# Optimization experiments

Hardware: AMD Instinct MI355X
Metric: run time of the kernel (lower is better)

Reference implementation:

```python
import jax, jax.numpy as jnp
import numpy as np

B, C, H, W = 16, 256, 32, 32
NUM_LAYERS = 30
OUT = 16  # sqrt(out_channels)
EPS = 1e-5


def setup_inputs() -> dict:
    key = jax.random.key(0)
    k1, k2, k3 = jax.random.split(key, 3)
    x = jax.random.normal(k1, (B, C, H, W), dtype=jnp.float32)
    # delta_t ~ small positive values (module inits ~N(0.01, 0.005))
    delta_t = jax.random.uniform(k2, (NUM_LAYERS, 1), dtype=jnp.float32) * 0.02
    matrices = jax.random.normal(k3, (NUM_LAYERS, 1, 1, OUT, OUT), dtype=jnp.float32) * 0.1
    gamma = jnp.ones((H * W,), dtype=jnp.float32)   # BatchNorm2d weight, oc = i*i = H*W
    beta = jnp.zeros((H * W,), dtype=jnp.float32)   # BatchNorm2d bias
    return {"x": x, "delta_t": delta_t, "matrices": matrices, "gamma": gamma, "beta": beta}


def _bn_relu6(z, gamma, beta):
    # training-mode BatchNorm2d over channel axis 1 (channels = H*W), then ReLU6
    mean = jnp.mean(z, axis=(0, 2, 3), keepdims=True)
    var = jnp.mean(jnp.square(z - mean), axis=(0, 2, 3), keepdims=True)  # biased var
    zhat = (z - mean) * jax.lax.rsqrt(var + EPS)
    g = gamma.reshape(1, -1, 1, 1)
    b = beta.reshape(1, -1, 1, 1)
    return jnp.clip(zhat * g + b, 0.0, 6.0)


def reference(x, delta_t, matrices, gamma, beta):
    b, c, h, w = x.shape
    hw = h * w
    # feature_reshape: [B,C,H,W] -> [B,HW,C] -> [B,HW,out,out] (inn == out branch)
    x1 = x.reshape(b, c, hw).transpose(0, 2, 1).reshape(b, hw, OUT, OUT)
    dt = jnp.clip(delta_t, 0.0, 6.0)[:, 0]  # relu6(delta_t), shape [L]

    def step(y0, params):
        m, dtl = params  # m: [1,1,out,out] broadcasts elementwise against x1
        dydt = -y0 + _bn_relu6(y0 + m * x1, gamma, beta)
        return y0 + dtl * dydt, None

    y0, _ = jax.lax.scan(step, x1, (matrices, dt))
    # (y0 + x1): [B, HW, out, out] -> view [B,H,W,out*out] -> permute to [B,out*out,H,W]
    y = (y0 + x1).reshape(b, h, w, OUT * OUT).transpose(0, 3, 1, 2)
    return y
```

## Files before the change

kernel.cpp:

```cpp
#include <hip/hip_runtime.h>

typedef float v2f __attribute__((ext_vector_type(2)));
typedef float v4f __attribute__((ext_vector_type(4)));

#define HW      1024
#define NROWS   4096
#define NLAYERS 30
#define TPB     256

static __device__ __forceinline__ v2f pk_fma(v2f a, v2f b, v2f c) {
    v2f d; asm("v_pk_fma_f32 %0, %1, %2, %3" : "=v"(d) : "v"(a), "v"(b), "v"(c));
    return d;
}
static __device__ __forceinline__ v2f pk_add(v2f a, v2f b) {
    v2f d; asm("v_pk_add_f32 %0, %1, %2" : "=v"(d) : "v"(a), "v"(b));
    return d;
}

template <int CTRL, int RMASK>
__device__ __forceinline__ float dpp_add(float x) {
    int t = __builtin_amdgcn_update_dpp(0, __builtin_bit_cast(int, x),
                                        CTRL, RMASK, 0xf, true);
    return x + __builtin_bit_cast(float, t);
}
__device__ __forceinline__ float wave_sum64(float x) {
    x = dpp_add<0x111, 0xf>(x);
    x = dpp_add<0x112, 0xf>(x);
    x = dpp_add<0x114, 0xf>(x);
    x = dpp_add<0x118, 0xf>(x);
    x = dpp_add<0x142, 0xa>(x);
    x = dpp_add<0x143, 0xc>(x);
    return x;
}

__global__ __launch_bounds__(TPB) void txp64(const float* __restrict__ src,
                                             float* __restrict__ dst,
                                             int M, int N) {
    __shared__ float tile[64][65];
    const int n0 = blockIdx.x * 64;
    const int m0 = blockIdx.y * 64;
    const int tx = threadIdx.x & 63;
    const int ty = threadIdx.x >> 6;
#pragma unroll
    for (int i = 0; i < 16; ++i) {
        const int r = ty + 4 * i;
        tile[r][tx] = src[(size_t)(m0 + r) * N + n0 + tx];
    }
    __syncthreads();
#pragma unroll
    for (int i = 0; i < 16; ++i) {
        const int r = ty + 4 * i;
        dst[(size_t)(n0 + r) * M + m0 + tx] = tile[tx][r];
    }
}

__global__ __launch_bounds__(TPB, 4) void ode_z4w(
    float* ws, const float* __restrict__ delta_t,
    const float* __restrict__ matrices, const float* __restrict__ gamma,
    const float* __restrict__ beta) {

    const int p    = blockIdx.x;
    const int t    = threadIdx.x;
    const int wid  = t >> 6;
    const int lane = t & 63;
    const int c0   = (4 * t) & 255;
    float* row = ws + (size_t)p * NROWS;

    __shared__ float xs[NROWS];
    __shared__ __align__(16) v2f red[2][4];

    const float gp = gamma[p];
    const float bp = beta[p];

    v2f z[8];
    v2f s0 = {0.f, 0.f}, s1 = {0.f, 0.f}, q0 = {0.f, 0.f}, q1 = {0.f, 0.f};

    {
        const v4f m4 = *(const v4f*)(matrices + c0);
        const v2f mA = {m4.x, m4.y}, mB = {m4.z, m4.w};
#pragma unroll
        for (int j = 0; j < 4; ++j) {
            const v4f x4 = *(const v4f*)(row + 4 * t + 1024 * j);
            *(v4f*)&xs[4 * t + 1024 * j] = x4;
            const v2f xA = {x4.x, x4.y}, xB = {x4.z, x4.w};
            z[2 * j]     = pk_fma(mA, xA, xA);
            z[2 * j + 1] = pk_fma(mB, xB, xB);
            s0 = pk_add(s0, z[2 * j]);
            q0 = pk_fma(z[2 * j], z[2 * j], q0);
            s1 = pk_add(s1, z[2 * j + 1]);
            q1 = pk_fma(z[2 * j + 1], z[2 * j + 1], q1);
        }
        const v2f sv = pk_add(s0, s1);
        const v2f qv = pk_add(q0, q1);
        const float ss = wave_sum64(sv.x + sv.y);
        const float qq = wave_sum64(qv.x + qv.y);
        if (lane == 63) red[0][wid] = (v2f){ss, qq};
    }

    v4f   mqc = *(const v4f*)(matrices + c0);
    v4f   mqn = *(const v4f*)(matrices + 256 + c0);
    float dtc = delta_t[0];
    float dtn = delta_t[1];
    __syncthreads();

    for (int k = 0; k < NLAYERS - 1; ++k) {
        const int k2 = (k + 2 < NLAYERS) ? k + 2 : NLAYERS - 1;
        const v4f   mq2   = *(const v4f*)(matrices + k2 * 256 + c0);
        const float dt_nn = delta_t[k2];

        const int par = k & 1;
        const v4f r0 = *(const v4f*)&red[par][0];
        const v4f r1 = *(const v4f*)&red[par][2];
        const float S = (r0.x + r0.z) + (r1.x + r1.z);
        const float Q = (r0.y + r0.w) + (r1.y + r1.w);

        const float dtk  = __builtin_amdgcn_fmed3f(dtc, 0.0f, 6.0f);
        const float mean = S * (1.0f / 4096.0f);
        const float var  = fmaf(-mean, mean, Q * (1.0f / 4096.0f));
        const float rstd = rsqrtf(var + 1e-5f);
        const float g    = gp * rstd;
        const float b    = fmaf(-mean, g, bp);
        const float om   = 1.0f - dtk;
        const float gd   = g * dtk;
        const float bd   = b * dtk;
        const float hi   = 6.0f * dtk;
        const v2f gd2 = {gd, gd}, bd2 = {bd, bd};
        const v2f om2 = {om, om};
        const v2f omn = {-om, -om};
        const v2f mcA = {mqc.x, mqc.y}, mcB = {mqc.z, mqc.w};
        const v2f mnA = {mqn.x, mqn.y}, mnB = {mqn.z, mqn.w};
        const v2f dmA = pk_fma(omn, mcA, mnA);
        const v2f dmB = pk_fma(omn, mcB, mnB);

        s0 = (v2f){0.f, 0.f}; s1 = (v2f){0.f, 0.f};
        q0 = (v2f){0.f, 0.f}; q1 = (v2f){0.f, 0.f};

#pragma unroll
        for (int j = 0; j < 4; ++j) {
            const v4f x4 = *(const v4f*)&xs[4 * t + 1024 * j];
            const v2f xA = {x4.x, x4.y}, xB = {x4.z, x4.w};
            {
                const int e = 2 * j;
                v2f a = pk_fma(z[e], gd2, bd2);
                a.x = __builtin_amdgcn_fmed3f(a.x, 0.0f, hi);
                a.y = __builtin_amdgcn_fmed3f(a.y, 0.0f, hi);
                v2f u = pk_fma(dmA, xA, a);
                z[e] = pk_fma(om2, z[e], u);
                s0 = pk_add(s0, z[e]);
                q0 = pk_fma(z[e], z[e], q0);
            }
            {
                const int e = 2 * j + 1;
                v2f a = pk_fma(z[e], gd2, bd2);
                a.x = __builtin_amdgcn_fmed3f(a.x, 0.0f, hi);
                a.y = __builtin_amdgcn_fmed3f(a.y, 0.0f, hi);
                v2f u = pk_fma(dmB, xB, a);
                z[e] = pk_fma(om2, z[e], u);
                s1 = pk_add(s1, z[e]);
                q1 = pk_fma(z[e], z[e], q1);
            }
        }
        const v2f sv = pk_add(s0, s1);
        const v2f qv = pk_add(q0, q1);
        const float ss = wave_sum64(sv.x + sv.y);
        const float qq = wave_sum64(qv.x + qv.y);
        if (lane == 63) red[par ^ 1][wid] = (v2f){ss, qq};

        mqc = mqn; mqn = mq2; dtc = dtn; dtn = dt_nn;
        __syncthreads();
    }

    {
        const v4f r0 = *(const v4f*)&red[(NLAYERS - 1) & 1][0];
        const v4f r1 = *(const v4f*)&red[(NLAYERS - 1) & 1][2];
        const float S = (r0.x + r0.z) + (r1.x + r1.z);
        const float Q = (r0.y + r0.w) + (r1.y + r1.w);

        const float dtk  = __builtin_amdgcn_fmed3f(dtc, 0.0f, 6.0f);
        const float mean = S * (1.0f / 4096.0f);
        const float var  = fmaf(-mean, mean, Q * (1.0f / 4096.0f));
        const float rstd = rsqrtf(var + 1e-5f);
        const float g    = gp * rstd;
        const float b    = fmaf(-mean, g, bp);
        const float om   = 1.0f - dtk;
        const float gd   = g * dtk;
        const float bd   = b * dtk;
        const float hi   = 6.0f * dtk;
        const v2f gd2 = {gd, gd}, bd2 = {bd, bd};
        const v2f om2 = {om, om};
        const v2f omn = {-om, -om};
        const v2f one2 = {1.0f, 1.0f};
        const v2f mcA = {mqc.x, mqc.y}, mcB = {mqc.z, mqc.w};
        const v2f dmA = pk_fma(omn, mcA, one2);
        const v2f dmB = pk_fma(omn, mcB, one2);

#pragma unroll
        for (int j = 0; j < 4; ++j) {
            const v4f x4 = *(const v4f*)&xs[4 * t + 1024 * j];
            const v2f xA = {x4.x, x4.y}, xB = {x4.z, x4.w};
            v2f o0, o1;
            {
                const int e = 2 * j;
                v2f a = pk_fma(z[e], gd2, bd2);
                a.x = __builtin_amdgcn_fmed3f(a.x, 0.0f, hi);
                a.y = __builtin_amdgcn_fmed3f(a.y, 0.0f, hi);
                v2f u = pk_fma(dmA, xA, a);
                o0 = pk_fma(om2, z[e], u);
            }
            {
                const int e = 2 * j + 1;
                v2f a = pk_fma(z[e], gd2, bd2);
                a.x = __builtin_amdgcn_fmed3f(a.x, 0.0f, hi);
                a.y = __builtin_amdgcn_fmed3f(a.y, 0.0f, hi);
                v2f u = pk_fma(dmB, xB, a);
                o1 = pk_fma(om2, z[e], u);
            }
            v4f o4; o4.x = o0.x; o4.y = o0.y; o4.z = o1.x; o4.w = o1.y;
            *(v4f*)(row + 4 * t + 1024 * j) = o4;
        }
    }
}

__global__ __launch_bounds__(TPB) void ode_fused(const float* __restrict__ x,
                                                 const float* __restrict__ delta_t,
                                                 const float* __restrict__ matrices,
                                                 const float* __restrict__ gamma,
                                                 const float* __restrict__ beta,
                                                 float* __restrict__ out) {
    const int bid = blockIdx.x;
    const int p   = ((bid & 7) << 7) | (bid >> 3);
    const int t   = threadIdx.x;

    __shared__ float smat[(NLAYERS + 1) * 256];
    __shared__ float sdt[NLAYERS];
    __shared__ __align__(16) v2f red[2][4];

#pragma unroll
    for (int i = 0; i < NLAYERS; ++i)
        smat[i * 256 + t] = matrices[i * 256 + t];
    if (t < NLAYERS)
        sdt[t] = __builtin_amdgcn_fmed3f(delta_t[t], 0.0f, 6.0f);

    v2f x1[8], y[8];
#pragma unroll
    for (int k = 0; k < 8; ++k) {
        x1[k].x = x[(size_t)(t + 512 * k) * HW + p];
        x1[k].y = x[(size_t)(t + 512 * k + 256) * HW + p];
        y[k] = x1[k];
    }

    const float gp   = gamma[p];
    const float bp   = beta[p];
    const int   wid  = t >> 6;
    const int   lane = t & 63;

    __syncthreads();
    float m_cur = smat[t];

    for (int l = 0; l < NLAYERS; ++l) {
        const float dtl = sdt[l];
        const v2f m2    = {m_cur, m_cur};
        const v2f dt2   = {dtl, dtl};
        const v2f om2   = {1.0f - dtl, 1.0f - dtl};

        v2f z[8];
        v2f sA = {0.f, 0.f}, sB = {0.f, 0.f};
        v2f qA = {0.f, 0.f}, qB = {0.f, 0.f};
#pragma unroll
        for (int k = 0; k < 8; k += 2) {
            z[k]     = __builtin_elementwise_fma(m2, x1[k], y[k]);
            z[k + 1] = __builtin_elementwise_fma(m2, x1[k + 1], y[k + 1]);
            sA += z[k];
            sB += z[k + 1];
            qA = __builtin_elementwise_fma(z[k], z[k], qA);
            qB = __builtin_elementwise_fma(z[k + 1], z[k + 1], qB);
        }
#pragma unroll
        for (int k = 0; k < 8; ++k) y[k] *= om2;

        const v2f sv = sA + sB;
        const v2f qv = qA + qB;
        float s = wave_sum64(sv.x + sv.y);
        float q = wave_sum64(qv.x + qv.y);

        const int par = l & 1;
        if (lane == 63) { v2f w; w.x = s; w.y = q; red[par][wid] = w; }
        m_cur = smat[(l + 1) * 256 + t];
        __syncthreads();

        const float4 r0 = *(const float4*)&red[par][0];
        const float4 r1 = *(const float4*)&red[par][2];
        const float S  = (r0.x + r0.z) + (r1.x + r1.z);
        const float S2 = (r0.y + r0.w) + (r1.y + r1.w);

        const float mean = S * (1.0f / 4096.0f);
        const float var  = fmaf(-mean, mean, S2 * (1.0f / 4096.0f));
        const float rstd = rsqrtf(var + 1e-5f);
        const float g    = gp * rstd;
        const float bb   = fmaf(-mean, g, bp);
        const v2f g2 = {g, g}, b2 = {bb, bb};
        const v2f z0 = {0.f, 0.f}, s6 = {6.f, 6.f};
#pragma unroll
        for (int k = 0; k < 8; ++k) {
            v2f a = __builtin_elementwise_fma(z[k], g2, b2);
            a = __builtin_elementwise_max(a, z0);
            a = __builtin_elementwise_min(a, s6);
            y[k] = __builtin_elementwise_fma(dt2, a, y[k]);
        }
    }

#pragma unroll
    for (int k = 0; k < 8; ++k) {
        out[(size_t)(t + 512 * k) * HW + p]       = y[k].x + x1[k].x;
        out[(size_t)(t + 512 * k + 256) * HW + p] = y[k].y + x1[k].y;
    }
}

extern "C" void kernel_launch(void* const* d_in, const int* in_sizes, int n_in,
                              void* d_out, int out_size, void* d_ws, size_t ws_size,
                              hipStream_t stream) {
    const float* x        = (const float*)d_in[0];
    const float* delta_t  = (const float*)d_in[1];
    const float* matrices = (const float*)d_in[2];
    const float* gamma    = (const float*)d_in[3];
    const float* beta     = (const float*)d_in[4];
    float* out = (float*)d_out;

    const size_t need = (size_t)HW * NROWS * sizeof(float);
    if (d_ws != nullptr && ws_size >= need) {
        float* ws = (float*)d_ws;
        txp64<<<dim3(HW / 64, NROWS / 64), dim3(TPB), 0, stream>>>(x, ws, NROWS, HW);
        ode_z4w<<<dim3(HW), dim3(TPB), 0, stream>>>(ws, delta_t, matrices, gamma, beta);
        txp64<<<dim3(NROWS / 64, HW / 64), dim3(TPB), 0, stream>>>(ws, out, HW, NROWS);
    } else {
        ode_fused<<<dim3(HW), dim3(TPB), 0, stream>>>(x, delta_t, matrices, gamma, beta, out);
    }
}
```

Baseline: 119.7 us.

## Run each BN channel's ODE in a single wavefront with register-resident state

The per-channel ODE kernel now uses one 64-lane wavefront per channel instead of four waves. Each lane keeps 64 state values and 64 input values in registers rather than staging x in LDS. The batch-norm statistics are reduced with DPP plus readlane, which removes the per-layer __syncthreads and LDS exchange. The cost is a much larger register footprint and only 1024 single-wave blocks, so occupancy and latency hiding drop and per-lane serial work per layer is four times larger.

```diff
diff --git a/kernel.cpp b/kernel.cpp
--- a/kernel.cpp
+++ b/kernel.cpp
@@ -32,6 +32,10 @@
     x = dpp_add<0x143, 0xc>(x);
     return x;
 }
+__device__ __forceinline__ float bcast63(float x) {
+    return __builtin_bit_cast(float,
+        __builtin_amdgcn_readlane(__builtin_bit_cast(int, x), 63));
+}
 
 __global__ __launch_bounds__(TPB) void txp64(const float* __restrict__ src,
                                              float* __restrict__ dst,
@@ -54,35 +58,30 @@
     }
 }
 
-__global__ __launch_bounds__(TPB, 4) void ode_z4w(
-    float* ws, const float* __restrict__ delta_t,
+__global__ __launch_bounds__(64, 1) void ode_zreg(
+    float* __restrict__ ws, const float* __restrict__ delta_t,
     const float* __restrict__ matrices, const float* __restrict__ gamma,
     const float* __restrict__ beta) {
 
     const int p    = blockIdx.x;
-    const int t    = threadIdx.x;
-    const int wid  = t >> 6;
-    const int lane = t & 63;
-    const int c0   = (4 * t) & 255;
+    const int lane = threadIdx.x;
+    const int c0   = 4 * lane;
     float* row = ws + (size_t)p * NROWS;
-
-    __shared__ float xs[NROWS];
-    __shared__ __align__(16) v2f red[2][4];
 
     const float gp = gamma[p];
     const float bp = beta[p];
 
-    v2f z[8];
+    v4f xr[16];
+    v2f z[32];
     v2f s0 = {0.f, 0.f}, s1 = {0.f, 0.f}, q0 = {0.f, 0.f}, q1 = {0.f, 0.f};
 
     {
         const v4f m4 = *(const v4f*)(matrices + c0);
         const v2f mA = {m4.x, m4.y}, mB = {m4.z, m4.w};
 #pragma unroll
-        for (int j = 0; j < 4; ++j) {
-            const v4f x4 = *(const v4f*)(row + 4 * t + 1024 * j);
-            *(v4f*)&xs[4 * t + 1024 * j] = x4;
-            const v2f xA = {x4.x, x4.y}, xB = {x4.z, x4.w};
+        for (int j = 0; j < 16; ++j) {
+            xr[j] = *(const v4f*)(row + 4 * lane + 256 * j);
+            const v2f xA = {xr[j].x, xr[j].y}, xB = {xr[j].z, xr[j].w};
             z[2 * j]     = pk_fma(mA, xA, xA);
             z[2 * j + 1] = pk_fma(mB, xB, xB);
             s0 = pk_add(s0, z[2 * j]);
@@ -90,29 +89,27 @@
             s1 = pk_add(s1, z[2 * j + 1]);
             q1 = pk_fma(z[2 * j + 1], z[2 * j + 1], q1);
         }
-        const v2f sv = pk_add(s0, s1);
-        const v2f qv = pk_add(q0, q1);
-        const float ss = wave_sum64(sv.x + sv.y);
-        const float qq = wave_sum64(qv.x + qv.y);
-        if (lane == 63) red[0][wid] = (v2f){ss, qq};
     }
 
     v4f   mqc = *(const v4f*)(matrices + c0);
     v4f   mqn = *(const v4f*)(matrices + 256 + c0);
     float dtc = delta_t[0];
     float dtn = delta_t[1];
-    __syncthreads();
 
     for (int k = 0; k < NLAYERS - 1; ++k) {
+        asm volatile("" : "+v"(xr[0]), "+v"(xr[1]), "+v"(xr[2]), "+v"(xr[3]));
+        asm volatile("" : "+v"(xr[4]), "+v"(xr[5]), "+v"(xr[6]), "+v"(xr[7]));
+        asm volatile("" : "+v"(xr[8]), "+v"(xr[9]), "+v"(xr[10]), "+v"(xr[11]));
+        asm volatile("" : "+v"(xr[12]), "+v"(xr[13]), "+v"(xr[14]), "+v"(xr[15]));
+
         const int k2 = (k + 2 < NLAYERS) ? k + 2 : NLAYERS - 1;
         const v4f   mq2   = *(const v4f*)(matrices + k2 * 256 + c0);
         const float dt_nn = delta_t[k2];
 
-        const int par = k & 1;
-        const v4f r0 = *(const v4f*)&red[par][0];
-        const v4f r1 = *(const v4f*)&red[par][2];
-        const float S = (r0.x + r0.z) + (r1.x + r1.z);
-        const float Q = (r0.y + r0.w) + (r1.y + r1.w);
+        const v2f sv = pk_add(s0, s1);
+        const v2f qv = pk_add(q0, q1);
+        const float S = bcast63(wave_sum64(sv.x + sv.y));
+        const float Q = bcast63(wave_sum64(qv.x + qv.y));
 
         const float dtk  = __builtin_amdgcn_fmed3f(dtc, 0.0f, 6.0f);
         const float mean = S * (1.0f / 4096.0f);
@@ -136,9 +133,8 @@
         q0 = (v2f){0.f, 0.f}; q1 = (v2f){0.f, 0.f};
 
 #pragma unroll
-        for (int j = 0; j < 4; ++j) {
-            const v4f x4 = *(const v4f*)&xs[4 * t + 1024 * j];
-            const v2f xA = {x4.x, x4.y}, xB = {x4.z, x4.w};
+        for (int j = 0; j < 16; ++j) {
+            const v2f xA = {xr[j].x, xr[j].y}, xB = {xr[j].z, xr[j].w};
             {
                 const int e = 2 * j;
                 v2f a = pk_fma(z[e], gd2, bd2);
@@ -160,21 +156,15 @@
                 q1 = pk_fma(z[e], z[e], q1);
             }
         }
+
+        mqc = mqn; mqn = mq2; dtc = dtn; dtn = dt_nn;
+    }
+
+    {
         const v2f sv = pk_add(s0, s1);
         const v2f qv = pk_add(q0, q1);
-        const float ss = wave_sum64(sv.x + sv.y);
-        const float qq = wave_sum64(qv.x + qv.y);
-        if (lane == 63) red[par ^ 1][wid] = (v2f){ss, qq};
-
-        mqc = mqn; mqn = mq2; dtc = dtn; dtn = dt_nn;
-        __syncthreads();
-    }
-
-    {
-        const v4f r0 = *(const v4f*)&red[(NLAYERS - 1) & 1][0];
-        const v4f r1 = *(const v4f*)&red[(NLAYERS - 1) & 1][2];
-        const float S = (r0.x + r0.z) + (r1.x + r1.z);
-        const float Q = (r0.y + r0.w) + (r1.y + r1.w);
+        const float S = bcast63(wave_sum64(sv.x + sv.y));
+        const float Q = bcast63(wave_sum64(qv.x + qv.y));
 
         const float dtk  = __builtin_amdgcn_fmed3f(dtc, 0.0f, 6.0f);
         const float mean = S * (1.0f / 4096.0f);
@@ -195,28 +185,25 @@
         const v2f dmB = pk_fma(omn, mcB, one2);
 
 #pragma unroll
-        for (int j = 0; j < 4; ++j) {
-            const v4f x4 = *(const v4f*)&xs[4 * t + 1024 * j];
-            const v2f xA = {x4.x, x4.y}, xB = {x4.z, x4.w};
+        for (int j = 0; j < 16; ++j) {
+            const v2f xA = {xr[j].x, xr[j].y}, xB = {xr[j].z, xr[j].w};
             v2f o0, o1;
             {
-                const int e = 2 * j;
-                v2f a = pk_fma(z[e], gd2, bd2);
+                v2f a = pk_fma(z[2 * j], gd2, bd2);
                 a.x = __builtin_amdgcn_fmed3f(a.x, 0.0f, hi);
                 a.y = __builtin_amdgcn_fmed3f(a.y, 0.0f, hi);
                 v2f u = pk_fma(dmA, xA, a);
-                o0 = pk_fma(om2, z[e], u);
+                o0 = pk_fma(om2, z[2 * j], u);
             }
             {
-                const int e = 2 * j + 1;
-                v2f a = pk_fma(z[e], gd2, bd2);
+                v2f a = pk_fma(z[2 * j + 1], gd2, bd2);
                 a.x = __builtin_amdgcn_fmed3f(a.x, 0.0f, hi);
                 a.y = __builtin_amdgcn_fmed3f(a.y, 0.0f, hi);
                 v2f u = pk_fma(dmB, xB, a);
-                o1 = pk_fma(om2, z[e], u);
+                o1 = pk_fma(om2, z[2 * j + 1], u);
             }
             v4f o4; o4.x = o0.x; o4.y = o0.y; o4.z = o1.x; o4.w = o1.y;
-            *(v4f*)(row + 4 * t + 1024 * j) = o4;
+            *(v4f*)(row + 4 * lane + 256 * j) = o4;
         }
     }
 }
@@ -330,7 +317,7 @@
     if (d_ws != nullptr && ws_size >= need) {
         float* ws = (float*)d_ws;
         txp64<<<dim3(HW / 64, NROWS / 64), dim3(TPB), 0, stream>>>(x, ws, NROWS, HW);
-        ode_z4w<<<dim3(HW), dim3(TPB), 0, stream>>>(ws, delta_t, matrices, gamma, beta);
+        ode_zreg<<<dim3(HW), dim3(64), 0, stream>>>(ws, delta_t, matrices, gamma, beta);
         txp64<<<dim3(NROWS / 64, HW / 64), dim3(TPB), 0, stream>>>(ws, out, HW, NROWS);
     } else {
         ode_fused<<<dim3(HW), dim3(TPB), 0, stream>>>(x, delta_t, matrices, gamma, beta, out);
```

Measured after the change: 111.5 us. 1.07x faster.

## Fuse output transpose into ODE kernel and keep inputs in registers

Applied to the files above, without the earlier changes.

The ODE kernel now writes its results directly to the output in transposed layout, so the second transpose kernel and its workspace round trip are gone. The per-thread input values are kept in registers instead of being staged through shared memory and re-read every layer. The block index is swizzled so that concurrently running blocks write neighbouring output columns. In exchange, the direct output stores are strided scalar writes that coalesce only across blocks, and the extra registers may lower occupancy.

```diff
diff --git a/kernel.cpp b/kernel.cpp
--- a/kernel.cpp
+++ b/kernel.cpp
@@ -54,24 +54,25 @@
     }
 }
 
-__global__ __launch_bounds__(TPB, 4) void ode_z4w(
-    float* ws, const float* __restrict__ delta_t,
+__global__ __launch_bounds__(TPB, 4) void ode_zr4(
+    const float* __restrict__ ws, const float* __restrict__ delta_t,
     const float* __restrict__ matrices, const float* __restrict__ gamma,
-    const float* __restrict__ beta) {
-
-    const int p    = blockIdx.x;
+    const float* __restrict__ beta, float* __restrict__ out) {
+
+    const int bid  = blockIdx.x;
+    const int p    = ((bid & 7) << 7) | (bid >> 3);
     const int t    = threadIdx.x;
     const int wid  = t >> 6;
     const int lane = t & 63;
     const int c0   = (4 * t) & 255;
-    float* row = ws + (size_t)p * NROWS;
-
-    __shared__ float xs[NROWS];
+    const float* row = ws + (size_t)p * NROWS;
+
     __shared__ __align__(16) v2f red[2][4];
 
     const float gp = gamma[p];
     const float bp = beta[p];
 
+    v4f xr[4];
     v2f z[8];
     v2f s0 = {0.f, 0.f}, s1 = {0.f, 0.f}, q0 = {0.f, 0.f}, q1 = {0.f, 0.f};
 
@@ -80,9 +81,8 @@
         const v2f mA = {m4.x, m4.y}, mB = {m4.z, m4.w};
 #pragma unroll
         for (int j = 0; j < 4; ++j) {
-            const v4f x4 = *(const v4f*)(row + 4 * t + 1024 * j);
-            *(v4f*)&xs[4 * t + 1024 * j] = x4;
-            const v2f xA = {x4.x, x4.y}, xB = {x4.z, x4.w};
+            xr[j] = *(const v4f*)(row + 4 * t + 1024 * j);
+            const v2f xA = {xr[j].x, xr[j].y}, xB = {xr[j].z, xr[j].w};
             z[2 * j]     = pk_fma(mA, xA, xA);
             z[2 * j + 1] = pk_fma(mB, xB, xB);
             s0 = pk_add(s0, z[2 * j]);
@@ -137,8 +137,7 @@
 
 #pragma unroll
         for (int j = 0; j < 4; ++j) {
-            const v4f x4 = *(const v4f*)&xs[4 * t + 1024 * j];
-            const v2f xA = {x4.x, x4.y}, xB = {x4.z, x4.w};
+            const v2f xA = {xr[j].x, xr[j].y}, xB = {xr[j].z, xr[j].w};
             {
                 const int e = 2 * j;
                 v2f a = pk_fma(z[e], gd2, bd2);
@@ -194,29 +193,30 @@
         const v2f dmA = pk_fma(omn, mcA, one2);
         const v2f dmB = pk_fma(omn, mcB, one2);
 
+        float* op = out + (size_t)(4 * t) * HW + p;
 #pragma unroll
         for (int j = 0; j < 4; ++j) {
-            const v4f x4 = *(const v4f*)&xs[4 * t + 1024 * j];
-            const v2f xA = {x4.x, x4.y}, xB = {x4.z, x4.w};
+            const v2f xA = {xr[j].x, xr[j].y}, xB = {xr[j].z, xr[j].w};
             v2f o0, o1;
             {
-                const int e = 2 * j;
-                v2f a = pk_fma(z[e], gd2, bd2);
+                v2f a = pk_fma(z[2 * j], gd2, bd2);
                 a.x = __builtin_amdgcn_fmed3f(a.x, 0.0f, hi);
                 a.y = __builtin_amdgcn_fmed3f(a.y, 0.0f, hi);
                 v2f u = pk_fma(dmA, xA, a);
-                o0 = pk_fma(om2, z[e], u);
+                o0 = pk_fma(om2, z[2 * j], u);
             }
             {
-                const int e = 2 * j + 1;
-                v2f a = pk_fma(z[e], gd2, bd2);
+                v2f a = pk_fma(z[2 * j + 1], gd2, bd2);
                 a.x = __builtin_amdgcn_fmed3f(a.x, 0.0f, hi);
                 a.y = __builtin_amdgcn_fmed3f(a.y, 0.0f, hi);
                 v2f u = pk_fma(dmB, xB, a);
-                o1 = pk_fma(om2, z[e], u);
+                o1 = pk_fma(om2, z[2 * j + 1], u);
             }
-            v4f o4; o4.x = o0.x; o4.y = o0.y; o4.z = o1.x; o4.w = o1.y;
-            *(v4f*)(row + 4 * t + 1024 * j) = o4;
+            const size_t base = (size_t)(1024 * j) * HW;
+            op[base]                  = o0.x;
+            op[base + HW]             = o0.y;
+            op[base + 2 * (size_t)HW] = o1.x;
+            op[base + 3 * (size_t)HW] = o1.y;
         }
     }
 }
@@ -330,8 +330,7 @@
     if (d_ws != nullptr && ws_size >= need) {
         float* ws = (float*)d_ws;
         txp64<<<dim3(HW / 64, NROWS / 64), dim3(TPB), 0, stream>>>(x, ws, NROWS, HW);
-        ode_z4w<<<dim3(HW), dim3(TPB), 0, stream>>>(ws, delta_t, matrices, gamma, beta);
-        txp64<<<dim3(NROWS / 64, HW / 64), dim3(TPB), 0, stream>>>(ws, out, HW, NROWS);
+        ode_zr4<<<dim3(HW), dim3(TPB), 0, stream>>>(ws, delta_t, matrices, gamma, beta, out);
     } else {
         ode_fused<<<dim3(HW), dim3(TPB), 0, stream>>>(x, delta_t, matrices, gamma, beta, out);
     }
```

Measured after the change: 129.0 us. 1.08x slower.
